# Kernel tuning notes

Measured on AMD Instinct MI355X. Metric: run time of the kernel, lower is better.

Reference implementation:

```python
import jax, jax.numpy as jnp
import numpy as np

N_NODES = 100000
SIG_DIM = 64
N_ADJ = 1600000
N_QUERY = 262144


def setup_inputs() -> dict:
    key = jax.random.key(0)
    k1, k2, k3, k4, k5 = jax.random.split(key, 5)
    x = jax.random.normal(k1, (N_NODES, SIG_DIM), dtype=jnp.float32)
    x = x / jnp.linalg.norm(x, axis=1, keepdims=True)  # F.normalize(p=2, dim=1)
    node_weight = jax.random.uniform(k2, (N_NODES,), dtype=jnp.float32)
    edges = jax.random.randint(k3, (2, N_QUERY), 0, N_NODES)
    adj_row = jnp.sort(jax.random.randint(k4, (N_ADJ,), 0, N_NODES))
    adj_col = jax.random.randint(k5, (N_ADJ,), 0, N_NODES)
    return {
        "x": x,
        "node_weight": node_weight,
        "edges": edges,
        "adj_row": adj_row,
        "adj_col": adj_col,
        "num_nodes": N_NODES,
    }


def reference(x, node_weight, edges, adj_row, adj_col, num_nodes):
    # node signatures scaled by node weight
    xw = x * node_weight[:, None]                      # [N, D]

    seg = lambda vals: jax.ops.segment_sum(vals, adj_row, num_segments=num_nodes)

    # SpMM propagation: (A @ x)[i] = sum_{j in N(i)} x[j]
    one_hop = seg(xw[adj_col])                          # [N, D]
    deg = seg(jnp.ones_like(adj_row, dtype=xw.dtype))   # [N]
    two_iter = seg(one_hop[adj_col])                    # [N, D]

    # combine mode
    two_hop = two_iter - one_hop - xw
    deg2 = jnp.maximum(seg(deg[adj_col]) - deg - 1.0, 0.0)

    row, col = edges[0], edges[1]
    x_u_1 = one_hop[row]
    x_v_1 = one_hop[col]
    x_u_2 = two_hop[row]
    x_v_2 = two_hop[col]

    dot = lambda a, b: (a * b).sum(axis=-1)

    deg_u = deg[row]
    deg_v = deg[col]
    deg_u_2 = deg2[row]
    deg_v_2 = deg2[col]

    count_1_1 = dot(x_u_1, x_v_1)
    count_1_2 = dot(x_u_1, x_v_2)
    count_2_1 = dot(x_u_2, x_v_1)
    count_2_2 = dot(x_u_2, x_v_2)
    count_1_inf = deg_u + deg_v - 2 * count_1_1 - count_1_2 - count_2_1
    count_2_inf = deg_u_2 + deg_v_2 - 2 * count_2_2 - count_1_2 - count_2_1

    x_u_iter = two_iter[row]
    x_v_iter = two_iter[col]
    x_u = xw[row]
    x_v = xw[col]
    comb_count_1_2 = dot(x_u_1, x_v_iter)
    comb_count_2_1 = dot(x_u_iter, x_v_1)
    comb_count_2_2 = dot(x_u_iter - deg_u[:, None] * x_u,
                         x_v_iter - deg_v[:, None] * x_v)
    comb_count_self_1_2 = dot(x_u_1, x_u_iter)
    comb_count_self_2_1 = dot(x_v_1, x_v_iter)

    features = jnp.stack([
        count_1_1, count_1_2, count_2_1, count_2_2,
        count_1_inf, count_2_inf,
        comb_count_1_2, comb_count_2_1, comb_count_2_2,
        comb_count_self_1_2, comb_count_self_2_1,
        deg_u, deg_v, deg_u_2, deg_v_2,
    ], axis=1)                                          # [E, 15]
    return features
```

## Files before the change

kernel.cpp:

```cpp
#include <hip/hip_runtime.h>


#define D 64

typedef unsigned int uint32;
typedef _Float16 h2 __attribute__((ext_vector_type(2)));

union U32H2 { uint32 u; h2 h; };
__device__ __forceinline__ h2 u_as_h2(uint32 u) { U32H2 t; t.u = u; return t.h; }

__device__ __forceinline__ uint32 pack2(float a, float b) {
    uint32 ua = __float_as_uint(a);
    ua += 0x7fffu + ((ua >> 16) & 1u);
    uint32 ub = __float_as_uint(b);
    ub += 0x7fffu + ((ub >> 16) & 1u);
    return (ua >> 16) | (ub & 0xffff0000u);
}
__device__ __forceinline__ float lo2f(uint32 u) { return __uint_as_float(u << 16); }
__device__ __forceinline__ float hi2f(uint32 u) { return __uint_as_float(u & 0xffff0000u); }

__device__ __forceinline__ uint32 enc1(float v) {
    float a = fabsf(v);
    uint32 s = (__float_as_uint(v) >> 24) & 0x80u;
    if (a >= 448.f) return s | 0x7Eu;
    if (a < 0.015625f) {
        uint32 m = (uint32)rintf(a * 512.f);
        return (m > 7u) ? (s | 0x08u) : (s | m);
    }
    uint32 b = __float_as_uint(a);
    b += 0x7FFFFu + ((b >> 20) & 1u);
    uint32 m3 = (b >> 20) & 7u;
    int e4 = (int)(b >> 23) - 127 + 7;
    if (e4 > 15) return s | 0x7Eu;
    return s | ((uint32)e4 << 3) | m3;
}

__device__ __forceinline__ void dec8(uint32 u, uint32& pe, uint32& po) {
    uint32 se = (u << 8) & 0x80008000u;
    uint32 ue = u & 0x007f007fu;
    pe = ((ue << 7) + 0x08000800u) | se;
    uint32 so = u & 0x80008000u;
    uint32 uo = (u >> 8) & 0x007f007fu;
    po = ((uo << 7) + 0x08000800u) | so;
}

#define RED_GRP(v)  { v += __shfl_xor(v, 1, 64); v += __shfl_xor(v, 2, 64);  v += __shfl_xor(v, 4, 64);  }

__global__ void __launch_bounds__(256) prep_kernel(const float4* __restrict__ x,
                                                   const float* __restrict__ w,
                                                   uint2* __restrict__ xw,
                                                   const int* __restrict__ adj_row,
                                                   int* __restrict__ row_ptr,
                                                   int n8, int n, int nadj, int xw_blocks) {
    if ((int)blockIdx.x < xw_blocks) {
        int i = blockIdx.x * blockDim.x + threadIdx.x;
        if (i >= n8) return;
        float s = w[i >> 3] * 64.f;
        float4 a = x[i * 2], b = x[i * 2 + 1];
        uint32 w0 = enc1(a.x * s) | (enc1(a.z * s) << 8)
                  | (enc1(a.y * s) << 16) | (enc1(a.w * s) << 24);
        uint32 w1 = enc1(b.x * s) | (enc1(b.z * s) << 8)
                  | (enc1(b.y * s) << 16) | (enc1(b.w * s) << 24);
        xw[i] = make_uint2(w0, w1);
    } else {
        int i = (blockIdx.x - xw_blocks) * blockDim.x + threadIdx.x;
        if (i > n) return;
        int lo = 0, hi = nadj;
        while (lo < hi) {
            int mid = (lo + hi) >> 1;
            if (adj_row[mid] < i) lo = mid + 1; else hi = mid;
        }
        row_ptr[i] = lo;
    }
}

__global__ void __launch_bounds__(256) spmm1_kernel(const uint2* __restrict__ src,
                                                    const int* __restrict__ row_ptr,
                                                    const int* __restrict__ adj_col,
                                                    uint4* __restrict__ dst,
                                                    float* __restrict__ degout,
                                                    int n) {
    int lane = threadIdx.x & 63;
    int sub = lane & 7;
    int node = blockIdx.x * 32 + (threadIdx.x >> 6) * 8 + (lane >> 3);
    if (node >= n) return;
    int start = row_ptr[node], end = row_ptr[node + 1];
    int deg_n = end - start;
    h2 acc0 = u_as_h2(0u), acc1 = u_as_h2(0u), acc2 = u_as_h2(0u), acc3 = u_as_h2(0u);
    int gbase = lane & 56;
    const int* colp = adj_col + start;
    int base = 0;
    for (; base + 8 <= deg_n; base += 8) {
        int idx = colp[base + sub];
#pragma unroll
        for (int i = 0; i < 8; ++i) {
            int c = __shfl(idx, gbase + i, 64);
            uint2 qv = src[(size_t)c * 8 + sub];
            uint32 pe, po;
            dec8(qv.x, pe, po);
            acc0 += u_as_h2(pe); acc1 += u_as_h2(po);
            dec8(qv.y, pe, po);
            acc2 += u_as_h2(pe); acc3 += u_as_h2(po);
        }
    }
    if (base < deg_n) {
        int k = base + sub;
        int idx = (k < deg_n) ? colp[k] : 0;
#pragma unroll
        for (int i = 0; i < 8; ++i) {
            if (base + i < deg_n) {
                int c = __shfl(idx, gbase + i, 64);
                uint2 qv = src[(size_t)c * 8 + sub];
                uint32 pe, po;
                dec8(qv.x, pe, po);
                acc0 += u_as_h2(pe); acc1 += u_as_h2(po);
                dec8(qv.y, pe, po);
                acc2 += u_as_h2(pe); acc3 += u_as_h2(po);
            }
        }
    }
    uint4 o;
    o.x = pack2((float)acc0.x, (float)acc0.y);
    o.y = pack2((float)acc1.x, (float)acc1.y);
    o.z = pack2((float)acc2.x, (float)acc2.y);
    o.w = pack2((float)acc3.x, (float)acc3.y);
    dst[(size_t)node * 8 + sub] = o;
    if (sub == 0) degout[node] = (float)deg_n;
}

__global__ void __launch_bounds__(256) spmm2_kernel(const uint4* __restrict__ src,
                                                    const int* __restrict__ row_ptr,
                                                    const int* __restrict__ adj_col,
                                                    const float* __restrict__ degv,
                                                    uint4* __restrict__ dst,
                                                    float2* __restrict__ degpair,
                                                    int n) {
    int lane = threadIdx.x & 63;
    int sub = lane & 7;
    int node = blockIdx.x * 32 + (threadIdx.x >> 6) * 8 + (lane >> 3);
    if (node >= n) return;
    int start = row_ptr[node], end = row_ptr[node + 1];
    int deg_n = end - start;
    float a0 = 0.f, a1 = 0.f, a2 = 0.f, a3 = 0.f,
          a4 = 0.f, a5 = 0.f, a6 = 0.f, a7 = 0.f;
    float dsum = 0.f;
    int gbase = lane & 56;
    const int* colp = adj_col + start;
    int base = 0;
    for (; base + 8 <= deg_n; base += 8) {
        int idx = colp[base + sub];
        dsum += degv[idx];
#pragma unroll
        for (int i = 0; i < 8; ++i) {
            int c = __shfl(idx, gbase + i, 64);
            uint4 qv = src[(size_t)c * 8 + sub];
            a0 += lo2f(qv.x); a1 += hi2f(qv.x);
            a2 += lo2f(qv.y); a3 += hi2f(qv.y);
            a4 += lo2f(qv.z); a5 += hi2f(qv.z);
            a6 += lo2f(qv.w); a7 += hi2f(qv.w);
        }
    }
    if (base < deg_n) {
        int k = base + sub;
        bool kv = k < deg_n;
        int idx = kv ? colp[k] : 0;
        if (kv) dsum += degv[idx];
#pragma unroll
        for (int i = 0; i < 8; ++i) {
            if (base + i < deg_n) {
                int c = __shfl(idx, gbase + i, 64);
                uint4 qv = src[(size_t)c * 8 + sub];
                a0 += lo2f(qv.x); a1 += hi2f(qv.x);
                a2 += lo2f(qv.y); a3 += hi2f(qv.y);
                a4 += lo2f(qv.z); a5 += hi2f(qv.z);
                a6 += lo2f(qv.w); a7 += hi2f(qv.w);
            }
        }
    }
    uint4 o;
    o.x = pack2(a0, a1); o.y = pack2(a2, a3);
    o.z = pack2(a4, a5); o.w = pack2(a6, a7);
    dst[(size_t)node * 8 + sub] = o;
    RED_GRP(dsum)
    if (sub == 0)
        degpair[node] = make_float2((float)deg_n,
                                    fmaxf(dsum - (float)deg_n - 1.0f, 0.0f));
}

__global__ void __launch_bounds__(256) edge_kernel(const int* __restrict__ edges,
                                                   const uint2* __restrict__ xw,
                                                   const uint4* __restrict__ h1,
                                                   const uint4* __restrict__ t2,
                                                   const float2* __restrict__ degpair,
                                                   float* __restrict__ out,
                                                   int E) {
    int t = blockIdx.x * blockDim.x + threadIdx.x;
    int q = t >> 3, sub = t & 7;
    if (q >= E) return;
    int u = edges[q], v = edges[E + q];
    uint2 pxu = xw[(size_t)u * 8 + sub], pxv = xw[(size_t)v * 8 + sub];
    uint4 phu = h1[(size_t)u * 8 + sub], phv = h1[(size_t)v * 8 + sub];
    uint4 ptu = t2[(size_t)u * 8 + sub], ptv = t2[(size_t)v * 8 + sub];
    float2 dpu = degpair[u], dpv = degpair[v];
    float du = dpu.x, du2 = dpu.y, dv = dpv.x, dv2 = dpv.y;

    float fxu[8], fxv[8], fhu[8], fhv[8], ftu[8], ftv[8];
    {
        uint32 pe, po;
        dec8(pxu.x, pe, po);
        h2 e = u_as_h2(pe), o_ = u_as_h2(po);
        fxu[0] = (float)e.x; fxu[1] = (float)e.y; fxu[2] = (float)o_.x; fxu[3] = (float)o_.y;
        dec8(pxu.y, pe, po);
        e = u_as_h2(pe); o_ = u_as_h2(po);
        fxu[4] = (float)e.x; fxu[5] = (float)e.y; fxu[6] = (float)o_.x; fxu[7] = (float)o_.y;
        dec8(pxv.x, pe, po);
        e = u_as_h2(pe); o_ = u_as_h2(po);
        fxv[0] = (float)e.x; fxv[1] = (float)e.y; fxv[2] = (float)o_.x; fxv[3] = (float)o_.y;
        dec8(pxv.y, pe, po);
        e = u_as_h2(pe); o_ = u_as_h2(po);
        fxv[4] = (float)e.x; fxv[5] = (float)e.y; fxv[6] = (float)o_.x; fxv[7] = (float)o_.y;
    }
    fhu[0]=lo2f(phu.x); fhu[1]=hi2f(phu.x); fhu[2]=lo2f(phu.y); fhu[3]=hi2f(phu.y);
    fhu[4]=lo2f(phu.z); fhu[5]=hi2f(phu.z); fhu[6]=lo2f(phu.w); fhu[7]=hi2f(phu.w);
    fhv[0]=lo2f(phv.x); fhv[1]=hi2f(phv.x); fhv[2]=lo2f(phv.y); fhv[3]=hi2f(phv.y);
    fhv[4]=lo2f(phv.z); fhv[5]=hi2f(phv.z); fhv[6]=lo2f(phv.w); fhv[7]=hi2f(phv.w);
    ftu[0]=lo2f(ptu.x); ftu[1]=hi2f(ptu.x); ftu[2]=lo2f(ptu.y); ftu[3]=hi2f(ptu.y);
    ftu[4]=lo2f(ptu.z); ftu[5]=hi2f(ptu.z); ftu[6]=lo2f(ptu.w); ftu[7]=hi2f(ptu.w);
    ftv[0]=lo2f(ptv.x); ftv[1]=hi2f(ptv.x); ftv[2]=lo2f(ptv.y); ftv[3]=hi2f(ptv.y);
    ftv[4]=lo2f(ptv.z); ftv[5]=hi2f(ptv.z); ftv[6]=lo2f(ptv.w); ftv[7]=hi2f(ptv.w);

    float c11 = 0.f, c12 = 0.f, c21 = 0.f, c22 = 0.f,
          cc12 = 0.f, cc21 = 0.f, cc22 = 0.f, cs12 = 0.f, cs21 = 0.f;
#pragma unroll
    for (int j = 0; j < 8; ++j) {
        float xu = fxu[j], xv = fxv[j];
        float hu = fhu[j], hv = fhv[j];
        float tu = ftu[j], tv = ftv[j];
        float h2u = tu - hu - xu, h2v = tv - hv - xv;
        float au = fmaf(-du, xu, tu), av = fmaf(-dv, xv, tv);
        c11  = fmaf(hu,  hv,  c11);
        c12  = fmaf(hu,  h2v, c12);
        c21  = fmaf(h2u, hv,  c21);
        c22  = fmaf(h2u, h2v, c22);
        cc12 = fmaf(hu,  tv,  cc12);
        cc21 = fmaf(tu,  hv,  cc21);
        cc22 = fmaf(au,  av,  cc22);
        cs12 = fmaf(hu,  tu,  cs12);
        cs21 = fmaf(hv,  tv,  cs21);
    }
    RED_GRP(c11) RED_GRP(c12) RED_GRP(c21) RED_GRP(c22)
    RED_GRP(cc12) RED_GRP(cc21) RED_GRP(cc22) RED_GRP(cs12) RED_GRP(cs21)

    if (sub == 0) {
        float* o = out + (size_t)q * 15;
        o[0]  = c11;
        o[1]  = c12;
        o[2]  = c21;
        o[3]  = c22;
        o[4]  = du + dv - 2.f * c11 - c12 - c21;
        o[5]  = du2 + dv2 - 2.f * c22 - c12 - c21;
        o[6]  = cc12;
        o[7]  = cc21;
        o[8]  = cc22;
        o[9]  = cs12;
        o[10] = cs21;
        o[11] = du;
        o[12] = dv;
        o[13] = du2;
        o[14] = dv2;
    }
}

extern "C" void kernel_launch(void* const* d_in, const int* in_sizes, int n_in,
                              void* d_out, int out_size, void* d_ws, size_t ws_size,
                              hipStream_t stream) {
    const float* x       = (const float*)d_in[0];
    const float* w       = (const float*)d_in[1];
    const int*   edges   = (const int*)d_in[2];
    const int*   adj_row = (const int*)d_in[3];
    const int*   adj_col = (const int*)d_in[4];

    const int N    = in_sizes[1];
    const int E    = in_sizes[2] / 2;
    const int NADJ = in_sizes[3];

    char* ws = (char*)d_ws;
    size_t off = 0;
    auto take = [&](size_t bytes) {
        void* p = ws + off;
        off = (off + bytes + 255) & ~(size_t)255;
        return p;
    };
    uint2*  xw      = (uint2*)take((size_t)N * 8 * sizeof(uint2));
    uint4*  one_hop = (uint4*)take((size_t)N * D * 2);
    uint4*  two_it  = (uint4*)take((size_t)N * D * 2);
    float*  deg     = (float*)take((size_t)N * sizeof(float));
    float2* degpair = (float2*)take((size_t)N * sizeof(float2));
    int*    row_ptr = (int*)take((size_t)(N + 1) * sizeof(int));
    (void)ws_size;

    float* out = (float*)d_out;

    {
        int n8 = N * 8;
        int xw_blocks = (n8 + 255) / 256;
        int rp_blocks = (N + 1 + 255) / 256;
        prep_kernel<<<xw_blocks + rp_blocks, 256, 0, stream>>>(
            (const float4*)x, w, xw, adj_row, row_ptr, n8, N, NADJ, xw_blocks);
    }
    spmm1_kernel<<<(N + 31) / 32, 256, 0, stream>>>(xw, row_ptr, adj_col, one_hop, deg, N);
    spmm2_kernel<<<(N + 31) / 32, 256, 0, stream>>>(one_hop, row_ptr, adj_col, deg,
                                                    two_it, degpair, N);
    edge_kernel<<<((size_t)E * 8 + 255) / 256, 256, 0, stream>>>(edges, xw, one_hop, two_it,
                                                                 degpair, out, E);
}
```

Before: 185.8 us.

## Unroll SpMM gathers, prefetch column indices, and stage edge outputs in LDS

spmm1 gains a 16-neighbor main loop that issues two independent gathers per step, to raise memory-level parallelism. spmm2 software-pipelines the column-index load so the next block's indices are fetched while the current block's gathers run. edge_kernel now writes its 15 features per edge into shared memory and then stores them as one contiguous, coalesced range per block, replacing the strided per-edge stores from a single lane. The costs are extra registers in the SpMM loops and a block-wide barrier in the edge kernel.

```diff
diff --git a/kernel.cpp b/kernel.cpp
--- a/kernel.cpp
+++ b/kernel.cpp
@@ -90,6 +90,26 @@
     int gbase = lane & 56;
     const int* colp = adj_col + start;
     int base = 0;
+    for (; base + 16 <= deg_n; base += 16) {
+        int idx0 = colp[base + sub];
+        int idx1 = colp[base + 8 + sub];
+#pragma unroll
+        for (int i = 0; i < 8; ++i) {
+            int c0 = __shfl(idx0, gbase + i, 64);
+            int c1 = __shfl(idx1, gbase + i, 64);
+            uint2 q0 = src[(size_t)c0 * 8 + sub];
+            uint2 q1 = src[(size_t)c1 * 8 + sub];
+            uint32 pe, po;
+            dec8(q0.x, pe, po);
+            acc0 += u_as_h2(pe); acc1 += u_as_h2(po);
+            dec8(q0.y, pe, po);
+            acc2 += u_as_h2(pe); acc3 += u_as_h2(po);
+            dec8(q1.x, pe, po);
+            acc0 += u_as_h2(pe); acc1 += u_as_h2(po);
+            dec8(q1.y, pe, po);
+            acc2 += u_as_h2(pe); acc3 += u_as_h2(po);
+        }
+    }
     for (; base + 8 <= deg_n; base += 8) {
         int idx = colp[base + sub];
 #pragma unroll
@@ -146,20 +166,32 @@
     float dsum = 0.f;
     int gbase = lane & 56;
     const int* colp = adj_col + start;
-    int base = 0;
-    for (; base + 8 <= deg_n; base += 8) {
-        int idx = colp[base + sub];
-        dsum += degv[idx];
-#pragma unroll
-        for (int i = 0; i < 8; ++i) {
-            int c = __shfl(idx, gbase + i, 64);
-            uint4 qv = src[(size_t)c * 8 + sub];
-            a0 += lo2f(qv.x); a1 += hi2f(qv.x);
-            a2 += lo2f(qv.y); a3 += hi2f(qv.y);
-            a4 += lo2f(qv.z); a5 += hi2f(qv.z);
-            a6 += lo2f(qv.w); a7 += hi2f(qv.w);
-        }
-    }
+
+#define SPMM2_BLK(IDX)                                                 \
+    {                                                                  \
+        dsum += degv[IDX];                                             \
+        _Pragma("unroll")                                              \
+        for (int i = 0; i < 8; ++i) {                                  \
+            int c = __shfl(IDX, gbase + i, 64);                        \
+            uint4 qv = src[(size_t)c * 8 + sub];                       \
+            a0 += lo2f(qv.x); a1 += hi2f(qv.x);                        \
+            a2 += lo2f(qv.y); a3 += hi2f(qv.y);                        \
+            a4 += lo2f(qv.z); a5 += hi2f(qv.z);                        \
+            a6 += lo2f(qv.w); a7 += hi2f(qv.w);                        \
+        }                                                              \
+    }
+
+    int nfull = deg_n >> 3;
+    if (nfull > 0) {
+        int idx = colp[sub];
+        for (int b = 1; b < nfull; ++b) {
+            int idxn = colp[b * 8 + sub];
+            SPMM2_BLK(idx)
+            idx = idxn;
+        }
+        SPMM2_BLK(idx)
+    }
+    int base = nfull * 8;
     if (base < deg_n) {
         int k = base + sub;
         bool kv = k < deg_n;
@@ -177,6 +209,7 @@
             }
         }
     }
+#undef SPMM2_BLK
     uint4 o;
     o.x = pack2(a0, a1); o.y = pack2(a2, a3);
     o.z = pack2(a4, a5); o.w = pack2(a6, a7);
@@ -194,80 +227,92 @@
                                                    const float2* __restrict__ degpair,
                                                    float* __restrict__ out,
                                                    int E) {
+    __shared__ float so[32 * 15];
     int t = blockIdx.x * blockDim.x + threadIdx.x;
     int q = t >> 3, sub = t & 7;
-    if (q >= E) return;
-    int u = edges[q], v = edges[E + q];
-    uint2 pxu = xw[(size_t)u * 8 + sub], pxv = xw[(size_t)v * 8 + sub];
-    uint4 phu = h1[(size_t)u * 8 + sub], phv = h1[(size_t)v * 8 + sub];
-    uint4 ptu = t2[(size_t)u * 8 + sub], ptv = t2[(size_t)v * 8 + sub];
-    float2 dpu = degpair[u], dpv = degpair[v];
-    float du = dpu.x, du2 = dpu.y, dv = dpv.x, dv2 = dpv.y;
-
-    float fxu[8], fxv[8], fhu[8], fhv[8], ftu[8], ftv[8];
-    {
-        uint32 pe, po;
-        dec8(pxu.x, pe, po);
-        h2 e = u_as_h2(pe), o_ = u_as_h2(po);
-        fxu[0] = (float)e.x; fxu[1] = (float)e.y; fxu[2] = (float)o_.x; fxu[3] = (float)o_.y;
-        dec8(pxu.y, pe, po);
-        e = u_as_h2(pe); o_ = u_as_h2(po);
-        fxu[4] = (float)e.x; fxu[5] = (float)e.y; fxu[6] = (float)o_.x; fxu[7] = (float)o_.y;
-        dec8(pxv.x, pe, po);
-        e = u_as_h2(pe); o_ = u_as_h2(po);
-        fxv[0] = (float)e.x; fxv[1] = (float)e.y; fxv[2] = (float)o_.x; fxv[3] = (float)o_.y;
-        dec8(pxv.y, pe, po);
-        e = u_as_h2(pe); o_ = u_as_h2(po);
-        fxv[4] = (float)e.x; fxv[5] = (float)e.y; fxv[6] = (float)o_.x; fxv[7] = (float)o_.y;
-    }
-    fhu[0]=lo2f(phu.x); fhu[1]=hi2f(phu.x); fhu[2]=lo2f(phu.y); fhu[3]=hi2f(phu.y);
-    fhu[4]=lo2f(phu.z); fhu[5]=hi2f(phu.z); fhu[6]=lo2f(phu.w); fhu[7]=hi2f(phu.w);
-    fhv[0]=lo2f(phv.x); fhv[1]=hi2f(phv.x); fhv[2]=lo2f(phv.y); fhv[3]=hi2f(phv.y);
-    fhv[4]=lo2f(phv.z); fhv[5]=hi2f(phv.z); fhv[6]=lo2f(phv.w); fhv[7]=hi2f(phv.w);
-    ftu[0]=lo2f(ptu.x); ftu[1]=hi2f(ptu.x); ftu[2]=lo2f(ptu.y); ftu[3]=hi2f(ptu.y);
-    ftu[4]=lo2f(ptu.z); ftu[5]=hi2f(ptu.z); ftu[6]=lo2f(ptu.w); ftu[7]=hi2f(ptu.w);
-    ftv[0]=lo2f(ptv.x); ftv[1]=hi2f(ptv.x); ftv[2]=lo2f(ptv.y); ftv[3]=hi2f(ptv.y);
-    ftv[4]=lo2f(ptv.z); ftv[5]=hi2f(ptv.z); ftv[6]=lo2f(ptv.w); ftv[7]=hi2f(ptv.w);
-
-    float c11 = 0.f, c12 = 0.f, c21 = 0.f, c22 = 0.f,
-          cc12 = 0.f, cc21 = 0.f, cc22 = 0.f, cs12 = 0.f, cs21 = 0.f;
-#pragma unroll
-    for (int j = 0; j < 8; ++j) {
-        float xu = fxu[j], xv = fxv[j];
-        float hu = fhu[j], hv = fhv[j];
-        float tu = ftu[j], tv = ftv[j];
-        float h2u = tu - hu - xu, h2v = tv - hv - xv;
-        float au = fmaf(-du, xu, tu), av = fmaf(-dv, xv, tv);
-        c11  = fmaf(hu,  hv,  c11);
-        c12  = fmaf(hu,  h2v, c12);
-        c21  = fmaf(h2u, hv,  c21);
-        c22  = fmaf(h2u, h2v, c22);
-        cc12 = fmaf(hu,  tv,  cc12);
-        cc21 = fmaf(tu,  hv,  cc21);
-        cc22 = fmaf(au,  av,  cc22);
-        cs12 = fmaf(hu,  tu,  cs12);
-        cs21 = fmaf(hv,  tv,  cs21);
-    }
-    RED_GRP(c11) RED_GRP(c12) RED_GRP(c21) RED_GRP(c22)
-    RED_GRP(cc12) RED_GRP(cc21) RED_GRP(cc22) RED_GRP(cs12) RED_GRP(cs21)
-
-    if (sub == 0) {
-        float* o = out + (size_t)q * 15;
-        o[0]  = c11;
-        o[1]  = c12;
-        o[2]  = c21;
-        o[3]  = c22;
-        o[4]  = du + dv - 2.f * c11 - c12 - c21;
-        o[5]  = du2 + dv2 - 2.f * c22 - c12 - c21;
-        o[6]  = cc12;
-        o[7]  = cc21;
-        o[8]  = cc22;
-        o[9]  = cs12;
-        o[10] = cs21;
-        o[11] = du;
-        o[12] = dv;
-        o[13] = du2;
-        o[14] = dv2;
+    bool valid = q < E;
+    if (valid) {
+        int u = edges[q], v = edges[E + q];
+        uint2 pxu = xw[(size_t)u * 8 + sub], pxv = xw[(size_t)v * 8 + sub];
+        uint4 phu = h1[(size_t)u * 8 + sub], phv = h1[(size_t)v * 8 + sub];
+        uint4 ptu = t2[(size_t)u * 8 + sub], ptv = t2[(size_t)v * 8 + sub];
+        float2 dpu = degpair[u], dpv = degpair[v];
+        float du = dpu.x, du2 = dpu.y, dv = dpv.x, dv2 = dpv.y;
+
+        float fxu[8], fxv[8], fhu[8], fhv[8], ftu[8], ftv[8];
+        {
+            uint32 pe, po;
+            dec8(pxu.x, pe, po);
+            h2 e = u_as_h2(pe), o_ = u_as_h2(po);
+            fxu[0] = (float)e.x; fxu[1] = (float)e.y; fxu[2] = (float)o_.x; fxu[3] = (float)o_.y;
+            dec8(pxu.y, pe, po);
+            e = u_as_h2(pe); o_ = u_as_h2(po);
+            fxu[4] = (float)e.x; fxu[5] = (float)e.y; fxu[6] = (float)o_.x; fxu[7] = (float)o_.y;
+            dec8(pxv.x, pe, po);
+            e = u_as_h2(pe); o_ = u_as_h2(po);
+            fxv[0] = (float)e.x; fxv[1] = (float)e.y; fxv[2] = (float)o_.x; fxv[3] = (float)o_.y;
+            dec8(pxv.y, pe, po);
+            e = u_as_h2(pe); o_ = u_as_h2(po);
+            fxv[4] = (float)e.x; fxv[5] = (float)e.y; fxv[6] = (float)o_.x; fxv[7] = (float)o_.y;
+        }
+        fhu[0]=lo2f(phu.x); fhu[1]=hi2f(phu.x); fhu[2]=lo2f(phu.y); fhu[3]=hi2f(phu.y);
+        fhu[4]=lo2f(phu.z); fhu[5]=hi2f(phu.z); fhu[6]=lo2f(phu.w); fhu[7]=hi2f(phu.w);
+        fhv[0]=lo2f(phv.x); fhv[1]=hi2f(phv.x); fhv[2]=lo2f(phv.y); fhv[3]=hi2f(phv.y);
+        fhv[4]=lo2f(phv.z); fhv[5]=hi2f(phv.z); fhv[6]=lo2f(phv.w); fhv[7]=hi2f(phv.w);
+        ftu[0]=lo2f(ptu.x); ftu[1]=hi2f(ptu.x); ftu[2]=lo2f(ptu.y); ftu[3]=hi2f(ptu.y);
+        ftu[4]=lo2f(ptu.z); ftu[5]=hi2f(ptu.z); ftu[6]=lo2f(ptu.w); ftu[7]=hi2f(ptu.w);
+        ftv[0]=lo2f(ptv.x); ftv[1]=hi2f(ptv.x); ftv[2]=lo2f(ptv.y); ftv[3]=hi2f(ptv.y);
+        ftv[4]=lo2f(ptv.z); ftv[5]=hi2f(ptv.z); ftv[6]=lo2f(ptv.w); ftv[7]=hi2f(ptv.w);
+
+        float c11 = 0.f, c12 = 0.f, c21 = 0.f, c22 = 0.f,
+              cc12 = 0.f, cc21 = 0.f, cc22 = 0.f, cs12 = 0.f, cs21 = 0.f;
+#pragma unroll
+        for (int j = 0; j < 8; ++j) {
+            float xu = fxu[j], xv = fxv[j];
+            float hu = fhu[j], hv = fhv[j];
+            float tu = ftu[j], tv = ftv[j];
+            float h2u = tu - hu - xu, h2v = tv - hv - xv;
+            float au = fmaf(-du, xu, tu), av = fmaf(-dv, xv, tv);
+            c11  = fmaf(hu,  hv,  c11);
+            c12  = fmaf(hu,  h2v, c12);
+            c21  = fmaf(h2u, hv,  c21);
+            c22  = fmaf(h2u, h2v, c22);
+            cc12 = fmaf(hu,  tv,  cc12);
+            cc21 = fmaf(tu,  hv,  cc21);
+            cc22 = fmaf(au,  av,  cc22);
+            cs12 = fmaf(hu,  tu,  cs12);
+            cs21 = fmaf(hv,  tv,  cs21);
+        }
+        RED_GRP(c11) RED_GRP(c12) RED_GRP(c21) RED_GRP(c22)
+        RED_GRP(cc12) RED_GRP(cc21) RED_GRP(cc22) RED_GRP(cs12) RED_GRP(cs21)
+
+        if (sub == 0) {
+            float* o = so + (threadIdx.x >> 3) * 15;
+            o[0]  = c11;
+            o[1]  = c12;
+            o[2]  = c21;
+            o[3]  = c22;
+            o[4]  = du + dv - 2.f * c11 - c12 - c21;
+            o[5]  = du2 + dv2 - 2.f * c22 - c12 - c21;
+            o[6]  = cc12;
+            o[7]  = cc21;
+            o[8]  = cc22;
+            o[9]  = cs12;
+            o[10] = cs21;
+            o[11] = du;
+            o[12] = dv;
+            o[13] = du2;
+            o[14] = dv2;
+        }
+    }
+    __syncthreads();
+    int eb = blockIdx.x * 32;
+    if (eb < E) {
+        int nval = E - eb; if (nval > 32) nval = 32;
+        int nflt = nval * 15;
+        size_t obase = (size_t)eb * 15;
+        for (int k = threadIdx.x; k < nflt; k += 256)
+            out[obase + k] = so[k];
     }
 }
 
```

Measured after the change: 190.9 us. 2.7% more time.

## Batch gathers in SpMM kernels and stage edge outputs through shared memory

Applied to the files above, without the earlier changes.

In both SpMM kernels the eight neighbour-row loads per chunk are now issued together before any decode or accumulate, which exposes more memory-level parallelism. Both kernels also get a minimum-occupancy hint in their launch bounds. The edge kernel now writes its 15 features per edge into shared memory and then stores them to global memory as coalesced contiguous words. The added __syncthreads and higher register pressure from holding eight loads could reduce occupancy or conflict with the launch-bounds hint.

```diff
diff --git a/kernel.cpp b/kernel.cpp
--- a/kernel.cpp
+++ b/kernel.cpp
@@ -74,12 +74,12 @@
     }
 }
 
-__global__ void __launch_bounds__(256) spmm1_kernel(const uint2* __restrict__ src,
-                                                    const int* __restrict__ row_ptr,
-                                                    const int* __restrict__ adj_col,
-                                                    uint4* __restrict__ dst,
-                                                    float* __restrict__ degout,
-                                                    int n) {
+__global__ void __launch_bounds__(256, 8) spmm1_kernel(const uint2* __restrict__ src,
+                                                       const int* __restrict__ row_ptr,
+                                                       const int* __restrict__ adj_col,
+                                                       uint4* __restrict__ dst,
+                                                       float* __restrict__ degout,
+                                                       int n) {
     int lane = threadIdx.x & 63;
     int sub = lane & 7;
     int node = blockIdx.x * 32 + (threadIdx.x >> 6) * 8 + (lane >> 3);
@@ -92,16 +92,32 @@
     int base = 0;
     for (; base + 8 <= deg_n; base += 8) {
         int idx = colp[base + sub];
-#pragma unroll
-        for (int i = 0; i < 8; ++i) {
-            int c = __shfl(idx, gbase + i, 64);
-            uint2 qv = src[(size_t)c * 8 + sub];
-            uint32 pe, po;
-            dec8(qv.x, pe, po);
-            acc0 += u_as_h2(pe); acc1 += u_as_h2(po);
-            dec8(qv.y, pe, po);
-            acc2 += u_as_h2(pe); acc3 += u_as_h2(po);
-        }
+        uint2 q0, q1, q2, q3, q4, q5, q6, q7;
+        {
+            int c0 = __shfl(idx, gbase + 0, 64);
+            int c1 = __shfl(idx, gbase + 1, 64);
+            int c2 = __shfl(idx, gbase + 2, 64);
+            int c3 = __shfl(idx, gbase + 3, 64);
+            int c4 = __shfl(idx, gbase + 4, 64);
+            int c5 = __shfl(idx, gbase + 5, 64);
+            int c6 = __shfl(idx, gbase + 6, 64);
+            int c7 = __shfl(idx, gbase + 7, 64);
+            q0 = src[(size_t)c0 * 8 + sub];
+            q1 = src[(size_t)c1 * 8 + sub];
+            q2 = src[(size_t)c2 * 8 + sub];
+            q3 = src[(size_t)c3 * 8 + sub];
+            q4 = src[(size_t)c4 * 8 + sub];
+            q5 = src[(size_t)c5 * 8 + sub];
+            q6 = src[(size_t)c6 * 8 + sub];
+            q7 = src[(size_t)c7 * 8 + sub];
+        }
+        uint32 pe, po;
+#define S1_ACC(Q) \
+        dec8(Q.x, pe, po); acc0 += u_as_h2(pe); acc1 += u_as_h2(po); \
+        dec8(Q.y, pe, po); acc2 += u_as_h2(pe); acc3 += u_as_h2(po);
+        S1_ACC(q0) S1_ACC(q1) S1_ACC(q2) S1_ACC(q3)
+        S1_ACC(q4) S1_ACC(q5) S1_ACC(q6) S1_ACC(q7)
+#undef S1_ACC
     }
     if (base < deg_n) {
         int k = base + sub;
@@ -128,13 +144,13 @@
     if (sub == 0) degout[node] = (float)deg_n;
 }
 
-__global__ void __launch_bounds__(256) spmm2_kernel(const uint4* __restrict__ src,
-                                                    const int* __restrict__ row_ptr,
-                                                    const int* __restrict__ adj_col,
-                                                    const float* __restrict__ degv,
-                                                    uint4* __restrict__ dst,
-                                                    float2* __restrict__ degpair,
-                                                    int n) {
+__global__ void __launch_bounds__(256, 8) spmm2_kernel(const uint4* __restrict__ src,
+                                                       const int* __restrict__ row_ptr,
+                                                       const int* __restrict__ adj_col,
+                                                       const float* __restrict__ degv,
+                                                       uint4* __restrict__ dst,
+                                                       float2* __restrict__ degpair,
+                                                       int n) {
     int lane = threadIdx.x & 63;
     int sub = lane & 7;
     int node = blockIdx.x * 32 + (threadIdx.x >> 6) * 8 + (lane >> 3);
@@ -150,15 +166,33 @@
     for (; base + 8 <= deg_n; base += 8) {
         int idx = colp[base + sub];
         dsum += degv[idx];
-#pragma unroll
-        for (int i = 0; i < 8; ++i) {
-            int c = __shfl(idx, gbase + i, 64);
-            uint4 qv = src[(size_t)c * 8 + sub];
-            a0 += lo2f(qv.x); a1 += hi2f(qv.x);
-            a2 += lo2f(qv.y); a3 += hi2f(qv.y);
-            a4 += lo2f(qv.z); a5 += hi2f(qv.z);
-            a6 += lo2f(qv.w); a7 += hi2f(qv.w);
-        }
+        uint4 q0, q1, q2, q3, q4, q5, q6, q7;
+        {
+            int c0 = __shfl(idx, gbase + 0, 64);
+            int c1 = __shfl(idx, gbase + 1, 64);
+            int c2 = __shfl(idx, gbase + 2, 64);
+            int c3 = __shfl(idx, gbase + 3, 64);
+            int c4 = __shfl(idx, gbase + 4, 64);
+            int c5 = __shfl(idx, gbase + 5, 64);
+            int c6 = __shfl(idx, gbase + 6, 64);
+            int c7 = __shfl(idx, gbase + 7, 64);
+            q0 = src[(size_t)c0 * 8 + sub];
+            q1 = src[(size_t)c1 * 8 + sub];
+            q2 = src[(size_t)c2 * 8 + sub];
+            q3 = src[(size_t)c3 * 8 + sub];
+            q4 = src[(size_t)c4 * 8 + sub];
+            q5 = src[(size_t)c5 * 8 + sub];
+            q6 = src[(size_t)c6 * 8 + sub];
+            q7 = src[(size_t)c7 * 8 + sub];
+        }
+#define S2_ACC(Q) \
+        a0 += lo2f(Q.x); a1 += hi2f(Q.x); \
+        a2 += lo2f(Q.y); a3 += hi2f(Q.y); \
+        a4 += lo2f(Q.z); a5 += hi2f(Q.z); \
+        a6 += lo2f(Q.w); a7 += hi2f(Q.w);
+        S2_ACC(q0) S2_ACC(q1) S2_ACC(q2) S2_ACC(q3)
+        S2_ACC(q4) S2_ACC(q5) S2_ACC(q6) S2_ACC(q7)
+#undef S2_ACC
     }
     if (base < deg_n) {
         int k = base + sub;
@@ -194,80 +228,92 @@
                                                    const float2* __restrict__ degpair,
                                                    float* __restrict__ out,
                                                    int E) {
+    __shared__ float so[32 * 15];
     int t = blockIdx.x * blockDim.x + threadIdx.x;
     int q = t >> 3, sub = t & 7;
-    if (q >= E) return;
-    int u = edges[q], v = edges[E + q];
-    uint2 pxu = xw[(size_t)u * 8 + sub], pxv = xw[(size_t)v * 8 + sub];
-    uint4 phu = h1[(size_t)u * 8 + sub], phv = h1[(size_t)v * 8 + sub];
-    uint4 ptu = t2[(size_t)u * 8 + sub], ptv = t2[(size_t)v * 8 + sub];
-    float2 dpu = degpair[u], dpv = degpair[v];
-    float du = dpu.x, du2 = dpu.y, dv = dpv.x, dv2 = dpv.y;
-
-    float fxu[8], fxv[8], fhu[8], fhv[8], ftu[8], ftv[8];
-    {
-        uint32 pe, po;
-        dec8(pxu.x, pe, po);
-        h2 e = u_as_h2(pe), o_ = u_as_h2(po);
-        fxu[0] = (float)e.x; fxu[1] = (float)e.y; fxu[2] = (float)o_.x; fxu[3] = (float)o_.y;
-        dec8(pxu.y, pe, po);
-        e = u_as_h2(pe); o_ = u_as_h2(po);
-        fxu[4] = (float)e.x; fxu[5] = (float)e.y; fxu[6] = (float)o_.x; fxu[7] = (float)o_.y;
-        dec8(pxv.x, pe, po);
-        e = u_as_h2(pe); o_ = u_as_h2(po);
-        fxv[0] = (float)e.x; fxv[1] = (float)e.y; fxv[2] = (float)o_.x; fxv[3] = (float)o_.y;
-        dec8(pxv.y, pe, po);
-        e = u_as_h2(pe); o_ = u_as_h2(po);
-        fxv[4] = (float)e.x; fxv[5] = (float)e.y; fxv[6] = (float)o_.x; fxv[7] = (float)o_.y;
-    }
-    fhu[0]=lo2f(phu.x); fhu[1]=hi2f(phu.x); fhu[2]=lo2f(phu.y); fhu[3]=hi2f(phu.y);
-    fhu[4]=lo2f(phu.z); fhu[5]=hi2f(phu.z); fhu[6]=lo2f(phu.w); fhu[7]=hi2f(phu.w);
-    fhv[0]=lo2f(phv.x); fhv[1]=hi2f(phv.x); fhv[2]=lo2f(phv.y); fhv[3]=hi2f(phv.y);
-    fhv[4]=lo2f(phv.z); fhv[5]=hi2f(phv.z); fhv[6]=lo2f(phv.w); fhv[7]=hi2f(phv.w);
-    ftu[0]=lo2f(ptu.x); ftu[1]=hi2f(ptu.x); ftu[2]=lo2f(ptu.y); ftu[3]=hi2f(ptu.y);
-    ftu[4]=lo2f(ptu.z); ftu[5]=hi2f(ptu.z); ftu[6]=lo2f(ptu.w); ftu[7]=hi2f(ptu.w);
-    ftv[0]=lo2f(ptv.x); ftv[1]=hi2f(ptv.x); ftv[2]=lo2f(ptv.y); ftv[3]=hi2f(ptv.y);
-    ftv[4]=lo2f(ptv.z); ftv[5]=hi2f(ptv.z); ftv[6]=lo2f(ptv.w); ftv[7]=hi2f(ptv.w);
-
-    float c11 = 0.f, c12 = 0.f, c21 = 0.f, c22 = 0.f,
-          cc12 = 0.f, cc21 = 0.f, cc22 = 0.f, cs12 = 0.f, cs21 = 0.f;
+    bool valid = q < E;
+    if (valid) {
+        int u = edges[q], v = edges[E + q];
+        uint2 pxu = xw[(size_t)u * 8 + sub], pxv = xw[(size_t)v * 8 + sub];
+        uint4 phu = h1[(size_t)u * 8 + sub], phv = h1[(size_t)v * 8 + sub];
+        uint4 ptu = t2[(size_t)u * 8 + sub], ptv = t2[(size_t)v * 8 + sub];
+        float2 dpu = degpair[u], dpv = degpair[v];
+        float du = dpu.x, du2 = dpu.y, dv = dpv.x, dv2 = dpv.y;
+
+        float fxu[8], fxv[8], fhu[8], fhv[8], ftu[8], ftv[8];
+        {
+            uint32 pe, po;
+            dec8(pxu.x, pe, po);
+            h2 e = u_as_h2(pe), o_ = u_as_h2(po);
+            fxu[0] = (float)e.x; fxu[1] = (float)e.y; fxu[2] = (float)o_.x; fxu[3] = (float)o_.y;
+            dec8(pxu.y, pe, po);
+            e = u_as_h2(pe); o_ = u_as_h2(po);
+            fxu[4] = (float)e.x; fxu[5] = (float)e.y; fxu[6] = (float)o_.x; fxu[7] = (float)o_.y;
+            dec8(pxv.x, pe, po);
+            e = u_as_h2(pe); o_ = u_as_h2(po);
+            fxv[0] = (float)e.x; fxv[1] = (float)e.y; fxv[2] = (float)o_.x; fxv[3] = (float)o_.y;
+            dec8(pxv.y, pe, po);
+            e = u_as_h2(pe); o_ = u_as_h2(po);
+            fxv[4] = (float)e.x; fxv[5] = (float)e.y; fxv[6] = (float)o_.x; fxv[7] = (float)o_.y;
+        }
+        fhu[0]=lo2f(phu.x); fhu[1]=hi2f(phu.x); fhu[2]=lo2f(phu.y); fhu[3]=hi2f(phu.y);
+        fhu[4]=lo2f(phu.z); fhu[5]=hi2f(phu.z); fhu[6]=lo2f(phu.w); fhu[7]=hi2f(phu.w);
+        fhv[0]=lo2f(phv.x); fhv[1]=hi2f(phv.x); fhv[2]=lo2f(phv.y); fhv[3]=hi2f(phv.y);
+        fhv[4]=lo2f(phv.z); fhv[5]=hi2f(phv.z); fhv[6]=lo2f(phv.w); fhv[7]=hi2f(phv.w);
+        ftu[0]=lo2f(ptu.x); ftu[1]=hi2f(ptu.x); ftu[2]=lo2f(ptu.y); ftu[3]=hi2f(ptu.y);
+        ftu[4]=lo2f(ptu.z); ftu[5]=hi2f(ptu.z); ftu[6]=lo2f(ptu.w); ftu[7]=hi2f(ptu.w);
+        ftv[0]=lo2f(ptv.x); ftv[1]=hi2f(ptv.x); ftv[2]=lo2f(ptv.y); ftv[3]=hi2f(ptv.y);
+        ftv[4]=lo2f(ptv.z); ftv[5]=hi2f(ptv.z); ftv[6]=lo2f(ptv.w); ftv[7]=hi2f(ptv.w);
+
+        float c11 = 0.f, c12 = 0.f, c21 = 0.f, c22 = 0.f,
+              cc12 = 0.f, cc21 = 0.f, cc22 = 0.f, cs12 = 0.f, cs21 = 0.f;
 #pragma unroll
-    for (int j = 0; j < 8; ++j) {
-        float xu = fxu[j], xv = fxv[j];
-        float hu = fhu[j], hv = fhv[j];
-        float tu = ftu[j], tv = ftv[j];
-        float h2u = tu - hu - xu, h2v = tv - hv - xv;
-        float au = fmaf(-du, xu, tu), av = fmaf(-dv, xv, tv);
-        c11  = fmaf(hu,  hv,  c11);
-        c12  = fmaf(hu,  h2v, c12);
-        c21  = fmaf(h2u, hv,  c21);
-        c22  = fmaf(h2u, h2v, c22);
-        cc12 = fmaf(hu,  tv,  cc12);
-        cc21 = fmaf(tu,  hv,  cc21);
-        cc22 = fmaf(au,  av,  cc22);
-        cs12 = fmaf(hu,  tu,  cs12);
-        cs21 = fmaf(hv,  tv,  cs21);
-    }
-    RED_GRP(c11) RED_GRP(c12) RED_GRP(c21) RED_GRP(c22)
-    RED_GRP(cc12) RED_GRP(cc21) RED_GRP(cc22) RED_GRP(cs12) RED_GRP(cs21)
-
-    if (sub == 0) {
-        float* o = out + (size_t)q * 15;
-        o[0]  = c11;
-        o[1]  = c12;
-        o[2]  = c21;
-        o[3]  = c22;
-        o[4]  = du + dv - 2.f * c11 - c12 - c21;
-        o[5]  = du2 + dv2 - 2.f * c22 - c12 - c21;
-        o[6]  = cc12;
-        o[7]  = cc21;
-        o[8]  = cc22;
-        o[9]  = cs12;
-        o[10] = cs21;
-        o[11] = du;
-        o[12] = dv;
-        o[13] = du2;
-        o[14] = dv2;
+        for (int j = 0; j < 8; ++j) {
+            float xu = fxu[j], xv = fxv[j];
+            float hu = fhu[j], hv = fhv[j];
+            float tu = ftu[j], tv = ftv[j];
+            float h2u = tu - hu - xu, h2v = tv - hv - xv;
+            float au = fmaf(-du, xu, tu), av = fmaf(-dv, xv, tv);
+            c11  = fmaf(hu,  hv,  c11);
+            c12  = fmaf(hu,  h2v, c12);
+            c21  = fmaf(h2u, hv,  c21);
+            c22  = fmaf(h2u, h2v, c22);
+            cc12 = fmaf(hu,  tv,  cc12);
+            cc21 = fmaf(tu,  hv,  cc21);
+            cc22 = fmaf(au,  av,  cc22);
+            cs12 = fmaf(hu,  tu,  cs12);
+            cs21 = fmaf(hv,  tv,  cs21);
+        }
+        RED_GRP(c11) RED_GRP(c12) RED_GRP(c21) RED_GRP(c22)
+        RED_GRP(cc12) RED_GRP(cc21) RED_GRP(cc22) RED_GRP(cs12) RED_GRP(cs21)
+
+        if (sub == 0) {
+            float* o = so + (threadIdx.x >> 3) * 15;
+            o[0]  = c11;
+            o[1]  = c12;
+            o[2]  = c21;
+            o[3]  = c22;
+            o[4]  = du + dv - 2.f * c11 - c12 - c21;
+            o[5]  = du2 + dv2 - 2.f * c22 - c12 - c21;
+            o[6]  = cc12;
+            o[7]  = cc21;
+            o[8]  = cc22;
+            o[9]  = cs12;
+            o[10] = cs21;
+            o[11] = du;
+            o[12] = dv;
+            o[13] = du2;
+            o[14] = dv2;
+        }
+    }
+    __syncthreads();
+    int eb = blockIdx.x * 32;
+    if (eb < E) {
+        int nval = E - eb; if (nval > 32) nval = 32;
+        int nflt = nval * 15;
+        size_t obase = (size_t)eb * 15;
+        for (int k = threadIdx.x; k < nflt; k += 256)
+            out[obase + k] = so[k];
     }
 }
 
```

Measured after the change: 185.4 us. Within noise of the previous version (-0.2%).

## Partition SpMM gathers into source-range passes and stage edge outputs in LDS

Applied to the files above, without the earlier changes.

Both SpMM kernels now sweep the neighbor list several times, each pass gathering only neighbors whose index falls in one slice of the node range. The aim is to keep the gathered source working set small enough to stay resident in cache. The cost is re-reading column indices and extra branches on every pass. The edge kernel also stages its 15-float outputs in shared memory and writes them back cooperatively, so global stores are coalesced instead of one thread per edge issuing strided scalar writes.

```diff
diff --git a/kernel.cpp b/kernel.cpp
--- a/kernel.cpp
+++ b/kernel.cpp
@@ -2,6 +2,8 @@
 
 
 #define D 64
+#define NPASS1 2
+#define NPASS2 5
 
 typedef unsigned int uint32;
 typedef _Float16 h2 __attribute__((ext_vector_type(2)));
@@ -89,33 +91,39 @@
     h2 acc0 = u_as_h2(0u), acc1 = u_as_h2(0u), acc2 = u_as_h2(0u), acc3 = u_as_h2(0u);
     int gbase = lane & 56;
     const int* colp = adj_col + start;
-    int base = 0;
-    for (; base + 8 <= deg_n; base += 8) {
-        int idx = colp[base + sub];
-#pragma unroll
-        for (int i = 0; i < 8; ++i) {
-            int c = __shfl(idx, gbase + i, 64);
-            uint2 qv = src[(size_t)c * 8 + sub];
-            uint32 pe, po;
-            dec8(qv.x, pe, po);
-            acc0 += u_as_h2(pe); acc1 += u_as_h2(po);
-            dec8(qv.y, pe, po);
-            acc2 += u_as_h2(pe); acc3 += u_as_h2(po);
-        }
-    }
-    if (base < deg_n) {
-        int k = base + sub;
-        int idx = (k < deg_n) ? colp[k] : 0;
-#pragma unroll
-        for (int i = 0; i < 8; ++i) {
-            if (base + i < deg_n) {
+    int slice = (n + NPASS1 - 1) / NPASS1;
+    for (int p = 0; p < NPASS1; ++p) {
+        int rlo = p * slice, rhi = rlo + slice;
+        int base = 0;
+        for (; base + 8 <= deg_n; base += 8) {
+            int idx = colp[base + sub];
+#pragma unroll
+            for (int i = 0; i < 8; ++i) {
                 int c = __shfl(idx, gbase + i, 64);
-                uint2 qv = src[(size_t)c * 8 + sub];
-                uint32 pe, po;
-                dec8(qv.x, pe, po);
-                acc0 += u_as_h2(pe); acc1 += u_as_h2(po);
-                dec8(qv.y, pe, po);
-                acc2 += u_as_h2(pe); acc3 += u_as_h2(po);
+                if (c >= rlo && c < rhi) {
+                    uint2 qv = src[(size_t)c * 8 + sub];
+                    uint32 pe, po;
+                    dec8(qv.x, pe, po);
+                    acc0 += u_as_h2(pe); acc1 += u_as_h2(po);
+                    dec8(qv.y, pe, po);
+                    acc2 += u_as_h2(pe); acc3 += u_as_h2(po);
+                }
+            }
+        }
+        if (base < deg_n) {
+            int k = base + sub;
+            int idx = (k < deg_n) ? colp[k] : -1;
+#pragma unroll
+            for (int i = 0; i < 8; ++i) {
+                int c = __shfl(idx, gbase + i, 64);
+                if (c >= rlo && c < rhi) {
+                    uint2 qv = src[(size_t)c * 8 + sub];
+                    uint32 pe, po;
+                    dec8(qv.x, pe, po);
+                    acc0 += u_as_h2(pe); acc1 += u_as_h2(po);
+                    dec8(qv.y, pe, po);
+                    acc2 += u_as_h2(pe); acc3 += u_as_h2(po);
+                }
             }
         }
     }
@@ -146,34 +154,40 @@
     float dsum = 0.f;
     int gbase = lane & 56;
     const int* colp = adj_col + start;
-    int base = 0;
-    for (; base + 8 <= deg_n; base += 8) {
-        int idx = colp[base + sub];
-        dsum += degv[idx];
-#pragma unroll
-        for (int i = 0; i < 8; ++i) {
-            int c = __shfl(idx, gbase + i, 64);
-            uint4 qv = src[(size_t)c * 8 + sub];
-            a0 += lo2f(qv.x); a1 += hi2f(qv.x);
-            a2 += lo2f(qv.y); a3 += hi2f(qv.y);
-            a4 += lo2f(qv.z); a5 += hi2f(qv.z);
-            a6 += lo2f(qv.w); a7 += hi2f(qv.w);
-        }
-    }
-    if (base < deg_n) {
-        int k = base + sub;
-        bool kv = k < deg_n;
-        int idx = kv ? colp[k] : 0;
-        if (kv) dsum += degv[idx];
-#pragma unroll
-        for (int i = 0; i < 8; ++i) {
-            if (base + i < deg_n) {
+    int slice = (n + NPASS2 - 1) / NPASS2;
+    for (int p = 0; p < NPASS2; ++p) {
+        int rlo = p * slice, rhi = rlo + slice;
+        int base = 0;
+        for (; base + 8 <= deg_n; base += 8) {
+            int idx = colp[base + sub];
+            if (p == 0) dsum += degv[idx];
+#pragma unroll
+            for (int i = 0; i < 8; ++i) {
                 int c = __shfl(idx, gbase + i, 64);
-                uint4 qv = src[(size_t)c * 8 + sub];
-                a0 += lo2f(qv.x); a1 += hi2f(qv.x);
-                a2 += lo2f(qv.y); a3 += hi2f(qv.y);
-                a4 += lo2f(qv.z); a5 += hi2f(qv.z);
-                a6 += lo2f(qv.w); a7 += hi2f(qv.w);
+                if (c >= rlo && c < rhi) {
+                    uint4 qv = src[(size_t)c * 8 + sub];
+                    a0 += lo2f(qv.x); a1 += hi2f(qv.x);
+                    a2 += lo2f(qv.y); a3 += hi2f(qv.y);
+                    a4 += lo2f(qv.z); a5 += hi2f(qv.z);
+                    a6 += lo2f(qv.w); a7 += hi2f(qv.w);
+                }
+            }
+        }
+        if (base < deg_n) {
+            int k = base + sub;
+            bool kv = k < deg_n;
+            int idx = kv ? colp[k] : -1;
+            if (p == 0 && kv) dsum += degv[idx];
+#pragma unroll
+            for (int i = 0; i < 8; ++i) {
+                int c = __shfl(idx, gbase + i, 64);
+                if (c >= rlo && c < rhi) {
+                    uint4 qv = src[(size_t)c * 8 + sub];
+                    a0 += lo2f(qv.x); a1 += hi2f(qv.x);
+                    a2 += lo2f(qv.y); a3 += hi2f(qv.y);
+                    a4 += lo2f(qv.z); a5 += hi2f(qv.z);
+                    a6 += lo2f(qv.w); a7 += hi2f(qv.w);
+                }
             }
         }
     }
@@ -194,80 +208,92 @@
                                                    const float2* __restrict__ degpair,
                                                    float* __restrict__ out,
                                                    int E) {
+    __shared__ float so[32 * 15];
     int t = blockIdx.x * blockDim.x + threadIdx.x;
     int q = t >> 3, sub = t & 7;
-    if (q >= E) return;
-    int u = edges[q], v = edges[E + q];
-    uint2 pxu = xw[(size_t)u * 8 + sub], pxv = xw[(size_t)v * 8 + sub];
-    uint4 phu = h1[(size_t)u * 8 + sub], phv = h1[(size_t)v * 8 + sub];
-    uint4 ptu = t2[(size_t)u * 8 + sub], ptv = t2[(size_t)v * 8 + sub];
-    float2 dpu = degpair[u], dpv = degpair[v];
-    float du = dpu.x, du2 = dpu.y, dv = dpv.x, dv2 = dpv.y;
-
-    float fxu[8], fxv[8], fhu[8], fhv[8], ftu[8], ftv[8];
-    {
-        uint32 pe, po;
-        dec8(pxu.x, pe, po);
-        h2 e = u_as_h2(pe), o_ = u_as_h2(po);
-        fxu[0] = (float)e.x; fxu[1] = (float)e.y; fxu[2] = (float)o_.x; fxu[3] = (float)o_.y;
-        dec8(pxu.y, pe, po);
-        e = u_as_h2(pe); o_ = u_as_h2(po);
-        fxu[4] = (float)e.x; fxu[5] = (float)e.y; fxu[6] = (float)o_.x; fxu[7] = (float)o_.y;
-        dec8(pxv.x, pe, po);
-        e = u_as_h2(pe); o_ = u_as_h2(po);
-        fxv[0] = (float)e.x; fxv[1] = (float)e.y; fxv[2] = (float)o_.x; fxv[3] = (float)o_.y;
-        dec8(pxv.y, pe, po);
-        e = u_as_h2(pe); o_ = u_as_h2(po);
-        fxv[4] = (float)e.x; fxv[5] = (float)e.y; fxv[6] = (float)o_.x; fxv[7] = (float)o_.y;
-    }
-    fhu[0]=lo2f(phu.x); fhu[1]=hi2f(phu.x); fhu[2]=lo2f(phu.y); fhu[3]=hi2f(phu.y);
-    fhu[4]=lo2f(phu.z); fhu[5]=hi2f(phu.z); fhu[6]=lo2f(phu.w); fhu[7]=hi2f(phu.w);
-    fhv[0]=lo2f(phv.x); fhv[1]=hi2f(phv.x); fhv[2]=lo2f(phv.y); fhv[3]=hi2f(phv.y);
-    fhv[4]=lo2f(phv.z); fhv[5]=hi2f(phv.z); fhv[6]=lo2f(phv.w); fhv[7]=hi2f(phv.w);
-    ftu[0]=lo2f(ptu.x); ftu[1]=hi2f(ptu.x); ftu[2]=lo2f(ptu.y); ftu[3]=hi2f(ptu.y);
-    ftu[4]=lo2f(ptu.z); ftu[5]=hi2f(ptu.z); ftu[6]=lo2f(ptu.w); ftu[7]=hi2f(ptu.w);
-    ftv[0]=lo2f(ptv.x); ftv[1]=hi2f(ptv.x); ftv[2]=lo2f(ptv.y); ftv[3]=hi2f(ptv.y);
-    ftv[4]=lo2f(ptv.z); ftv[5]=hi2f(ptv.z); ftv[6]=lo2f(ptv.w); ftv[7]=hi2f(ptv.w);
-
-    float c11 = 0.f, c12 = 0.f, c21 = 0.f, c22 = 0.f,
-          cc12 = 0.f, cc21 = 0.f, cc22 = 0.f, cs12 = 0.f, cs21 = 0.f;
-#pragma unroll
-    for (int j = 0; j < 8; ++j) {
-        float xu = fxu[j], xv = fxv[j];
-        float hu = fhu[j], hv = fhv[j];
-        float tu = ftu[j], tv = ftv[j];
-        float h2u = tu - hu - xu, h2v = tv - hv - xv;
-        float au = fmaf(-du, xu, tu), av = fmaf(-dv, xv, tv);
-        c11  = fmaf(hu,  hv,  c11);
-        c12  = fmaf(hu,  h2v, c12);
-        c21  = fmaf(h2u, hv,  c21);
-        c22  = fmaf(h2u, h2v, c22);
-        cc12 = fmaf(hu,  tv,  cc12);
-        cc21 = fmaf(tu,  hv,  cc21);
-        cc22 = fmaf(au,  av,  cc22);
-        cs12 = fmaf(hu,  tu,  cs12);
-        cs21 = fmaf(hv,  tv,  cs21);
-    }
-    RED_GRP(c11) RED_GRP(c12) RED_GRP(c21) RED_GRP(c22)
-    RED_GRP(cc12) RED_GRP(cc21) RED_GRP(cc22) RED_GRP(cs12) RED_GRP(cs21)
-
-    if (sub == 0) {
-        float* o = out + (size_t)q * 15;
-        o[0]  = c11;
-        o[1]  = c12;
-        o[2]  = c21;
-        o[3]  = c22;
-        o[4]  = du + dv - 2.f * c11 - c12 - c21;
-        o[5]  = du2 + dv2 - 2.f * c22 - c12 - c21;
-        o[6]  = cc12;
-        o[7]  = cc21;
-        o[8]  = cc22;
-        o[9]  = cs12;
-        o[10] = cs21;
-        o[11] = du;
-        o[12] = dv;
-        o[13] = du2;
-        o[14] = dv2;
+    bool valid = q < E;
+    if (valid) {
+        int u = edges[q], v = edges[E + q];
+        uint2 pxu = xw[(size_t)u * 8 + sub], pxv = xw[(size_t)v * 8 + sub];
+        uint4 phu = h1[(size_t)u * 8 + sub], phv = h1[(size_t)v * 8 + sub];
+        uint4 ptu = t2[(size_t)u * 8 + sub], ptv = t2[(size_t)v * 8 + sub];
+        float2 dpu = degpair[u], dpv = degpair[v];
+        float du = dpu.x, du2 = dpu.y, dv = dpv.x, dv2 = dpv.y;
+
+        float fxu[8], fxv[8], fhu[8], fhv[8], ftu[8], ftv[8];
+        {
+            uint32 pe, po;
+            dec8(pxu.x, pe, po);
+            h2 e = u_as_h2(pe), o_ = u_as_h2(po);
+            fxu[0] = (float)e.x; fxu[1] = (float)e.y; fxu[2] = (float)o_.x; fxu[3] = (float)o_.y;
+            dec8(pxu.y, pe, po);
+            e = u_as_h2(pe); o_ = u_as_h2(po);
+            fxu[4] = (float)e.x; fxu[5] = (float)e.y; fxu[6] = (float)o_.x; fxu[7] = (float)o_.y;
+            dec8(pxv.x, pe, po);
+            e = u_as_h2(pe); o_ = u_as_h2(po);
+            fxv[0] = (float)e.x; fxv[1] = (float)e.y; fxv[2] = (float)o_.x; fxv[3] = (float)o_.y;
+            dec8(pxv.y, pe, po);
+            e = u_as_h2(pe); o_ = u_as_h2(po);
+            fxv[4] = (float)e.x; fxv[5] = (float)e.y; fxv[6] = (float)o_.x; fxv[7] = (float)o_.y;
+        }
+        fhu[0]=lo2f(phu.x); fhu[1]=hi2f(phu.x); fhu[2]=lo2f(phu.y); fhu[3]=hi2f(phu.y);
+        fhu[4]=lo2f(phu.z); fhu[5]=hi2f(phu.z); fhu[6]=lo2f(phu.w); fhu[7]=hi2f(phu.w);
+        fhv[0]=lo2f(phv.x); fhv[1]=hi2f(phv.x); fhv[2]=lo2f(phv.y); fhv[3]=hi2f(phv.y);
+        fhv[4]=lo2f(phv.z); fhv[5]=hi2f(phv.z); fhv[6]=lo2f(phv.w); fhv[7]=hi2f(phv.w);
+        ftu[0]=lo2f(ptu.x); ftu[1]=hi2f(ptu.x); ftu[2]=lo2f(ptu.y); ftu[3]=hi2f(ptu.y);
+        ftu[4]=lo2f(ptu.z); ftu[5]=hi2f(ptu.z); ftu[6]=lo2f(ptu.w); ftu[7]=hi2f(ptu.w);
+        ftv[0]=lo2f(ptv.x); ftv[1]=hi2f(ptv.x); ftv[2]=lo2f(ptv.y); ftv[3]=hi2f(ptv.y);
+        ftv[4]=lo2f(ptv.z); ftv[5]=hi2f(ptv.z); ftv[6]=lo2f(ptv.w); ftv[7]=hi2f(ptv.w);
+
+        float c11 = 0.f, c12 = 0.f, c21 = 0.f, c22 = 0.f,
+              cc12 = 0.f, cc21 = 0.f, cc22 = 0.f, cs12 = 0.f, cs21 = 0.f;
+#pragma unroll
+        for (int j = 0; j < 8; ++j) {
+            float xu = fxu[j], xv = fxv[j];
+            float hu = fhu[j], hv = fhv[j];
+            float tu = ftu[j], tv = ftv[j];
+            float h2u = tu - hu - xu, h2v = tv - hv - xv;
+            float au = fmaf(-du, xu, tu), av = fmaf(-dv, xv, tv);
+            c11  = fmaf(hu,  hv,  c11);
+            c12  = fmaf(hu,  h2v, c12);
+            c21  = fmaf(h2u, hv,  c21);
+            c22  = fmaf(h2u, h2v, c22);
+            cc12 = fmaf(hu,  tv,  cc12);
+            cc21 = fmaf(tu,  hv,  cc21);
+            cc22 = fmaf(au,  av,  cc22);
+            cs12 = fmaf(hu,  tu,  cs12);
+            cs21 = fmaf(hv,  tv,  cs21);
+        }
+        RED_GRP(c11) RED_GRP(c12) RED_GRP(c21) RED_GRP(c22)
+        RED_GRP(cc12) RED_GRP(cc21) RED_GRP(cc22) RED_GRP(cs12) RED_GRP(cs21)
+
+        if (sub == 0) {
+            float* o = so + (threadIdx.x >> 3) * 15;
+            o[0]  = c11;
+            o[1]  = c12;
+            o[2]  = c21;
+            o[3]  = c22;
+            o[4]  = du + dv - 2.f * c11 - c12 - c21;
+            o[5]  = du2 + dv2 - 2.f * c22 - c12 - c21;
+            o[6]  = cc12;
+            o[7]  = cc21;
+            o[8]  = cc22;
+            o[9]  = cs12;
+            o[10] = cs21;
+            o[11] = du;
+            o[12] = dv;
+            o[13] = du2;
+            o[14] = dv2;
+        }
+    }
+    __syncthreads();
+    int eb = blockIdx.x * 32;
+    if (eb < E) {
+        int nval = E - eb; if (nval > 32) nval = 32;
+        int nflt = nval * 15;
+        size_t obase = (size_t)eb * 15;
+        for (int k = threadIdx.x; k < nflt; k += 256)
+            out[obase + k] = so[k];
     }
 }
 
```

After: 266.3 us. 43.3% more time.
